# Kernel tuning notes

Hardware: AMD Instinct MI355X
Metric: run time of the kernel (lower is better)

## Reference

```python
import jax, jax.numpy as jnp
import numpy as np

# static architecture constants (match init_kwargs)
H, D, N_BASIS, MEM_LEN, QLEN = 16, 128, 1024, 512, 2048
RIDGE = 0.5
BASIS_SIGMAS = (0.005, 0.01)


def _gaussian_pdf(x, mu, sigma):
    return jnp.exp(-0.5 * ((x - mu) / sigma) ** 2) / (sigma * jnp.sqrt(2.0 * jnp.pi))


def _basis_params(n):
    # torch.meshgrid(linspace(0,1,n//2), sigmas, indexing='ij') then flatten
    m = jnp.linspace(0.0, 1.0, n // len(BASIS_SIGMAS)).astype(jnp.float32)
    mu = jnp.repeat(m, len(BASIS_SIGMAS))
    sigma = jnp.tile(jnp.asarray(BASIS_SIGMAS, jnp.float32), n // len(BASIS_SIGMAS))
    return mu, sigma


def _compute_G(l, b_mu, b_sigma, n):
    # padded linear positions on [-0.5+shift, 1.5-shift], l even -> 2l points
    shift = 1.0 / (2 * l)
    pos = jnp.linspace(-0.5 + shift, 1.5 - shift, 2 * l).astype(jnp.float32)
    F = _gaussian_pdf(pos[None, :], b_mu[:, None], b_sigma[:, None])  # [N, 2l]
    # G = F^T (F F^T + ridge I)^{-1}, then crop padding rows -> [l, N]
    G = jnp.linalg.solve(F @ F.T + RIDGE * jnp.eye(n, dtype=jnp.float32), F).T
    return G[l // 2: -(l // 2)]


def _forward(k, q, W_key, W_val, W_out, w_mu, w_sigma):
    d = H * D
    b_mu, b_sigma = _basis_params(N_BASIS)
    k = k[:, -512:, :]                                   # forward truncates memory
    l = k.shape[1]
    G = _compute_G(l, b_mu, b_sigma, N_BASIS)            # [l, N]
    # value_function: project signal onto basis coefficients B -> [1, N, d]
    B = jnp.einsum('bld,ln->bnd', k, G)
    keys = (B @ W_key.T).reshape(1, N_BASIS, H, D).transpose(0, 2, 1, 3)    # [1,H,N,D]
    values = (B @ W_val.T).reshape(1, N_BASIS, H, D).transpose(0, 2, 1, 3)  # [1,H,N,D]
    scores = jnp.einsum('bhqd,bhnd->bhqn', q / jnp.sqrt(jnp.float32(D)), keys)
    mu = jax.nn.sigmoid(scores @ w_mu)[..., None]                           # [1,H,Q,1]
    sigma_sq = jnp.maximum(jax.nn.softplus(scores @ w_sigma), 1e-4)[..., None]
    # continuous softmax over Gaussian RBFs: r_j = E_{t~N(mu,sigma_sq)}[psi_j(t)]
    # closed form: N(mu; b_mu_j, sigma_sq + b_sigma_j^2)
    r = _gaussian_pdf(b_mu, mu, jnp.sqrt(sigma_sq + b_sigma ** 2))          # [1,H,Q,N]
    context = jnp.einsum('bhqn,bhnd->bqhd', r, values).reshape(1, QLEN, d)
    return context @ W_out.T


def setup_inputs() -> dict:
    key = jax.random.key(0)
    ks = jax.random.split(key, 7)
    d = H * D
    s = 0.02
    return {
        'k': jax.random.normal(ks[0], (1, MEM_LEN, d), jnp.float32),
        'q': jax.random.normal(ks[1], (1, H, QLEN, D), jnp.float32),
        'W_key': jax.random.normal(ks[2], (d, d), jnp.float32) * s,
        'W_val': jax.random.normal(ks[3], (d, d), jnp.float32) * s,
        'W_out': jax.random.normal(ks[4], (d, d), jnp.float32) * s,
        'w_mu': jax.random.normal(ks[5], (N_BASIS,), jnp.float32) * s,
        'w_sigma': jax.random.normal(ks[6], (N_BASIS,), jnp.float32) * s,
        'new_doc': 1,
    }


def reference(k, q, W_key, W_val, W_out, w_mu, w_sigma, new_doc):
    # new_doc=True -> B_past/x_past reset, so only the fresh-memory path runs
    return _forward(k, q, W_key, W_val, W_out, w_mu, w_sigma)
```

## Files before the change

### kernel.cpp

```cpp
#include <hip/hip_runtime.h>
#include <hip/hip_bf16.h>
#include <vector>
#include <cmath>
#include <cstring>

using bf16 = __hip_bfloat16;
typedef short s16x8 __attribute__((ext_vector_type(8)));
typedef float f32x4 __attribute__((ext_vector_type(4)));

static constexpr int kH = 16, kD = 128, kNB = 1024, kML = 512, kQL = 2048, kDM = 2048;

#define VMB(N) do { asm volatile("s_waitcnt vmcnt(" #N ")" ::: "memory"); \
                    __builtin_amdgcn_s_barrier(); \
                    asm volatile("" ::: "memory"); } while (0)
#define VMLB(N) do { asm volatile("s_waitcnt vmcnt(" #N ") lgkmcnt(0)" ::: "memory"); \
                     __builtin_amdgcn_s_barrier(); \
                     asm volatile("" ::: "memory"); } while (0)
#define SWZ(c) ((c) ^ (((c) >> 4) & 3))

static void compute_Gt_host(float* Gt) {
  const int n = kNB, P = 2 * kML;
  std::vector<double> F((size_t)n * P), A((size_t)n * n), pos(P);
  const double shift = 1.0 / (double)P;
  const double p0 = -0.5 + shift, p1 = 1.5 - shift;
  for (int i = 0; i < P; i++) pos[i] = p0 + (p1 - p0) * (double)i / (double)(P - 1);
  const double c0 = 0.3989422804014327;
  std::vector<int> lo(n), hi(n);
  for (int b = 0; b < n; b++) {
    double mu = (double)(b >> 1) / 511.0;
    double sg = (b & 1) ? 0.01 : 0.005;
    double c = c0 / sg;
    double* Fb = &F[(size_t)b * P];
    for (int i = 0; i < P; i++) { double t = (pos[i] - mu) / sg; Fb[i] = c * exp(-0.5 * t * t); }
    int l = 0; while (l < P - 1 && pos[l] < mu - 14.0 * sg) l++;
    int h = P - 1; while (h > 0 && pos[h] > mu + 14.0 * sg) h--;
    lo[b] = l; hi[b] = h;
  }
  for (int i = 0; i < n; i++) {
    const double* fi = &F[(size_t)i * P];
    for (int j = 0; j <= i; j++) {
      const double* fj = &F[(size_t)j * P];
      int a = lo[i] > lo[j] ? lo[i] : lo[j];
      int b2 = hi[i] < hi[j] ? hi[i] : hi[j];
      double s = 0.0;
      for (int k2 = a; k2 <= b2; k2++) s += fi[k2] * fj[k2];
      A[(size_t)i * n + j] = s;
      if (i != j) A[(size_t)j * n + i] = s;
    }
    A[(size_t)i * n + i] += 0.5;
  }
  for (int j = 0; j < n; j++) {
    double* Aj = &A[(size_t)j * n];
    double d = Aj[j];
    for (int k2 = 0; k2 < j; k2++) d -= Aj[k2] * Aj[k2];
    d = std::sqrt(d); Aj[j] = d;
    double inv = 1.0 / d;
    for (int i = j + 1; i < n; i++) {
      double* Ai = &A[(size_t)i * n];
      double s = Ai[j];
      for (int k2 = 0; k2 < j; k2++) s -= Ai[k2] * Aj[k2];
      Ai[j] = s * inv;
    }
  }
  for (int i = 0; i < n; i++) {
    double* yi = &F[(size_t)i * P];
    const double* Ai = &A[(size_t)i * n];
    for (int k2 = 0; k2 < i; k2++) {
      double lik = Ai[k2];
      const double* yk = &F[(size_t)k2 * P];
      for (int t = 0; t < P; t++) yi[t] -= lik * yk[t];
    }
    double inv = 1.0 / Ai[i];
    for (int t = 0; t < P; t++) yi[t] *= inv;
  }
  for (int i = n - 1; i >= 0; i--) {
    double* xi = &F[(size_t)i * P];
    for (int k2 = i + 1; k2 < n; k2++) {
      double lki = A[(size_t)k2 * n + i];
      const double* xk = &F[(size_t)k2 * P];
      for (int t = 0; t < P; t++) xi[t] -= lki * xk[t];
    }
    double inv = 1.0 / A[(size_t)i * n + i];
    for (int t = 0; t < P; t++) xi[t] *= inv;
  }
  for (int b = 0; b < n; b++)
    for (int l = 0; l < kML; l++)
      Gt[(size_t)b * kML + l] = (float)F[(size_t)b * P + (kML / 2) + l];
}

static unsigned short f2bf_host(float x) {
  unsigned u; std::memcpy(&u, &x, 4);
  unsigned r = (u + 0x7FFFu + ((u >> 16) & 1u)) >> 16;
  return (unsigned short)r;
}
static float bf2f_host(unsigned short b) {
  unsigned u = ((unsigned)b) << 16; float f; std::memcpy(&f, &u, 4); return f;
}

namespace {
struct Init {
  float* d_GtTf = nullptr;
  unsigned short* d_Gth = nullptr;
  unsigned short* d_Gtl = nullptr;
  float* h_GtTf_pinned = nullptr;
  unsigned short* h_Gth_pinned = nullptr;
  unsigned short* h_Gtl_pinned = nullptr;
  std::vector<float> h_GtTf;
  std::vector<unsigned short> h_Gth, h_Gtl;
  Init() {
    std::vector<float> h_Gt((size_t)kNB * kML);
    compute_Gt_host(h_Gt.data());
    h_GtTf.resize(h_Gt.size());
    h_Gth.resize(h_Gt.size());
    h_Gtl.resize(h_Gt.size());
    for (int n = 0; n < kNB; n++)
      for (int l = 0; l < kML; l++) {
        float v = h_Gt[(size_t)n * kML + l];
        h_GtTf[(size_t)l * kNB + n] = v;
        unsigned short hb = f2bf_host(v);
        h_Gth[(size_t)n * kML + l] = hb;
        h_Gtl[(size_t)n * kML + l] = f2bf_host(v - bf2f_host(hb));
      }
    const size_t fb = h_Gt.size() * 4, bb = h_Gt.size() * 2;
    if (hipMalloc((void**)&d_GtTf, fb) == hipSuccess) {
      if (hipMemcpy(d_GtTf, h_GtTf.data(), fb, hipMemcpyHostToDevice) != hipSuccess) { hipFree(d_GtTf); d_GtTf = nullptr; }
    }
    if (hipMalloc((void**)&d_Gth, bb) == hipSuccess) {
      if (hipMemcpy(d_Gth, h_Gth.data(), bb, hipMemcpyHostToDevice) != hipSuccess) { hipFree(d_Gth); d_Gth = nullptr; }
    }
    if (hipMalloc((void**)&d_Gtl, bb) == hipSuccess) {
      if (hipMemcpy(d_Gtl, h_Gtl.data(), bb, hipMemcpyHostToDevice) != hipSuccess) { hipFree(d_Gtl); d_Gtl = nullptr; }
    }
    if (!d_GtTf && hipHostMalloc((void**)&h_GtTf_pinned, fb, 0) == hipSuccess)
      std::memcpy(h_GtTf_pinned, h_GtTf.data(), fb);
    if (!d_Gth && hipHostMalloc((void**)&h_Gth_pinned, bb, 0) == hipSuccess)
      std::memcpy(h_Gth_pinned, h_Gth.data(), bb);
    if (!d_Gtl && hipHostMalloc((void**)&h_Gtl_pinned, bb, 0) == hipSuccess)
      std::memcpy(h_Gtl_pinned, h_Gtl.data(), bb);
  }
};
Init g_init;
}

__device__ inline short f2bf(float x) {
  unsigned u = __float_as_uint(x);
  unsigned r = (u + 0x7FFFu + ((u >> 16) & 1u)) >> 16;
  return (short)r;
}
__device__ inline float bf2f(short b) {
  return __uint_as_float(((unsigned)(unsigned short)b) << 16);
}

__device__ inline void gload16(const void* g, void* l) {
  __builtin_amdgcn_global_load_lds(
      (__attribute__((address_space(1))) void*)(g),
      (__attribute__((address_space(3))) void*)(l),
      16, 0, 0);
}

__device__ inline int detect_local(const unsigned short* q) {
  int bad = 0;
  for (int i = threadIdx.x; i < 512; i += 256) {
    int e = (q[i] >> 7) & 0xFF;
    if (e >= 0x98) bad = 1;
  }
  __shared__ int s[256];
  s[threadIdx.x] = bad; __syncthreads();
  for (int k2 = 128; k2 > 0; k2 >>= 1) {
    if (threadIdx.x < k2) s[threadIdx.x] |= s[threadIdx.x + k2];
    __syncthreads();
  }
  return s[0];
}

__global__ __launch_bounds__(256) void prep_kernel(const unsigned short* __restrict__ q,
                                                   const void* __restrict__ kin,
                                                   const void* __restrict__ Wv,
                                                   short* __restrict__ k_bf,
                                                   short* __restrict__ Wv_bf,
                                                   float* __restrict__ bw,
                                                   int* __restrict__ flag) {
  const int f32 = detect_local(q);
  if (blockIdx.x == 0) {
    if (threadIdx.x == 0) *flag = f32;
    for (int i = threadIdx.x; i < 2 * kDM; i += 256) bw[i] = 0.f;
  }
  const void* src; short* dst; int i;
  if (blockIdx.x < 1024) { src = kin; dst = k_bf; i = blockIdx.x * 256 + threadIdx.x; }
  else { src = Wv; dst = Wv_bf; i = (blockIdx.x - 1024) * 256 + threadIdx.x; }
  if (f32) {
    float4 v = ((const float4*)src)[i];
    short4 o; o.x = f2bf(v.x); o.y = f2bf(v.y); o.z = f2bf(v.z); o.w = f2bf(v.w);
    ((short4*)dst)[i] = o;
  } else {
    ((short4*)dst)[i] = ((const short4*)src)[i];
  }
}

__global__ __launch_bounds__(256) void conv_bf16(const void* __restrict__ in,
                                                 short* __restrict__ out, int n4,
                                                 const int* __restrict__ flag) {
  int i = blockIdx.x * 256 + threadIdx.x;
  if (i >= n4) return;
  if (*flag) {
    float4 v = ((const float4*)in)[i];
    short4 o; o.x = f2bf(v.x); o.y = f2bf(v.y); o.z = f2bf(v.z); o.w = f2bf(v.w);
    ((short4*)out)[i] = o;
  } else {
    ((short4*)out)[i] = ((const short4*)in)[i];
  }
}

__global__ __launch_bounds__(256) void gw_kernel(const float* __restrict__ GtT,
                                                 const void* __restrict__ wmu,
                                                 const void* __restrict__ wsg,
                                                 float* __restrict__ gw,
                                                 const int* __restrict__ flag) {
  const bool f32 = (*flag != 0);
  const int l = blockIdx.x, t = threadIdx.x;
  const float* row = GtT + (long long)l * kNB;
  float a = 0.f, b = 0.f;
  for (int n = t; n < kNB; n += 256) {
    float g = row[n];
    float wm_ = f32 ? ((const float*)wmu)[n] : bf2f(((const short*)wmu)[n]);
    float ws_ = f32 ? ((const float*)wsg)[n] : bf2f(((const short*)wsg)[n]);
    a += g * wm_; b += g * ws_;
  }
  __shared__ float red[2][256];
  red[0][t] = a; red[1][t] = b;
  __syncthreads();
  for (int s = 128; s > 0; s >>= 1) {
    if (t < s) { red[0][t] += red[0][t + s]; red[1][t] += red[1][t + s]; }
    __syncthreads();
  }
  if (t == 0) { gw[l] = red[0][0]; gw[kML + l] = red[1][0]; }
}

__global__ __launch_bounds__(256) void bwk_kernel(const void* __restrict__ kin,
                                                  const float* __restrict__ gw,
                                                  float* __restrict__ bw,
                                                  const int* __restrict__ flag) {
  const bool f32 = (*flag != 0);
  int j = blockIdx.x * 256 + threadIdx.x;
  int l0 = blockIdx.y * 32;
  float a = 0.f, b = 0.f;
  for (int l = l0; l < l0 + 32; l++) {
    float kv = f32 ? ((const float*)kin)[(long long)l * kDM + j]
                   : bf2f(((const short*)kin)[(long long)l * kDM + j]);
    a += kv * gw[l]; b += kv * gw[kML + l];
  }
  atomicAdd(&bw[j], a);
  atomicAdd(&bw[kDM + j], b);
}

__global__ __launch_bounds__(256) void kw_kernel(const void* __restrict__ Wk,
                                                 const float* __restrict__ bw,
                                                 float* __restrict__ kw,
                                                 const int* __restrict__ flag) {
  const bool f32 = (*flag != 0);
  int i = blockIdx.x;
  float smu = 0.f, ssg = 0.f;
  if (f32) {
    const float* row = (const float*)Wk + (long long)i * kDM;
    for (int j = threadIdx.x; j < kDM; j += 256) { float w = row[j]; smu += w * bw[j]; ssg += w * bw[kDM + j]; }
  } else {
    const short* row = (const short*)Wk + (long long)i * kDM;
    for (int j = threadIdx.x; j < kDM; j += 256) { float w = bf2f(row[j]); smu += w * bw[j]; ssg += w * bw[kDM + j]; }
  }
  __shared__ float red[2][256];
  red[0][threadIdx.x] = smu; red[1][threadIdx.x] = ssg;
  __syncthreads();
  for (int s = 128; s > 0; s >>= 1) {
    if (threadIdx.x < (unsigned)s) {
      red[0][threadIdx.x] += red[0][threadIdx.x + s];
      red[1][threadIdx.x] += red[1][threadIdx.x + s];
    }
    __syncthreads();
  }
  if (threadIdx.x == 0) { kw[i] = red[0][0]; kw[kDM + i] = red[1][0]; }
}

template <int CSTORE>
__global__ __launch_bounds__(256) void mfma_gemm_bt(
    const short* __restrict__ A0, int lda, long long sA,
    const short* __restrict__ BT0, int ldb, long long sB,
    void* __restrict__ C0, int ldc, long long sC,
    int K, const int* __restrict__ flag) {
  __shared__ s16x8 lA[3][1024];
  __shared__ s16x8 lB[3][512];
  const short* A = A0 + (long long)blockIdx.z * sA;
  const short* BT = BT0 + (long long)blockIdx.z * sB;
  const int t = threadIdx.x;
  const int wave = t >> 6, lane = t & 63;
  const int quad = lane >> 4, l16 = lane & 15;
  const int wm = wave >> 1, wn = wave & 1;
  int m0, n0;
  if (gridDim.x == 32 && gridDim.y == 16) {
    const int bid = blockIdx.x + (blockIdx.y << 5);
    const int xcd = bid & 7, rank = bid >> 3;
    n0 = (((xcd & 3) << 3) + (rank & 7)) * 64;
    m0 = (((xcd >> 2) << 3) + (rank >> 3)) * 128;
  } else {
    m0 = blockIdx.y * 128; n0 = blockIdx.x * 64;
  }
  const int srow = lane & 15, skc = lane >> 4;
  auto stage = [&](int b, int kk) {
#pragma unroll
    for (int i = 0; i < 2; i++) {
      int sub = wave + i * 4;
      int m = sub * 16 + srow;
#pragma unroll
      for (int ks = 0; ks < 2; ks++)
        gload16(A + (long long)(m0 + m) * lda + kk + ks * 32 + skc * 8,
                &lA[b][ks * 512 + sub * 64]);
    }
    int mB = wave * 16 + srow;
#pragma unroll
    for (int ks = 0; ks < 2; ks++)
      gload16(BT + (long long)(n0 + mB) * ldb + kk + ks * 32 + skc * 8,
              &lB[b][ks * 256 + wave * 64]);
  };
  f32x4 acc[4][2];
  const f32x4 z = {0.f, 0.f, 0.f, 0.f};
#pragma unroll
  for (int i = 0; i < 4; i++)
#pragma unroll
    for (int j = 0; j < 2; j++) acc[i][j] = z;
  stage(0, 0);
  stage(1, 64);
  VMB(6);
  const int NT = K >> 6;
  int cur = 0, pf = 2;
  for (int tt = 0; tt < NT; ++tt) {
    const bool more = (tt + 2 < NT);
    if (more) stage(pf, (tt + 2) << 6);
#pragma unroll
    for (int ks = 0; ks < 2; ks++) {
      s16x8 af[4], bfr[2];
#pragma unroll
      for (int i = 0; i < 4; i++) af[i] = lA[cur][ks * 512 + (wm * 4 + i) * 64 + lane];
#pragma unroll
      for (int j = 0; j < 2; j++) bfr[j] = lB[cur][ks * 256 + (wn * 2 + j) * 64 + lane];
#pragma unroll
      for (int i = 0; i < 4; i++)
#pragma unroll
        for (int j = 0; j < 2; j++)
          acc[i][j] = __builtin_amdgcn_mfma_f32_16x16x32_bf16(af[i], bfr[j], acc[i][j], 0, 0, 0);
    }
    if (more) VMB(6); else VMB(0);
    cur = (cur == 2) ? 0 : cur + 1;
    pf = (pf == 2) ? 0 : pf + 1;
  }
  if (CSTORE == 0) {
    short* Cp = (short*)C0 + (long long)blockIdx.z * sC;
#pragma unroll
    for (int i = 0; i < 4; i++)
#pragma unroll
      for (int j = 0; j < 2; j++) {
        int gn = n0 + (wn * 2 + j) * 16 + l16;
#pragma unroll
        for (int rg = 0; rg < 4; rg++) {
          int gm = m0 + (wm * 4 + i) * 16 + quad * 4 + rg;
          Cp[(long long)gm * ldc + gn] = f2bf(acc[i][j][rg]);
        }
      }
  } else {
    if (*flag) {
      float* Cp = (float*)C0 + (long long)blockIdx.z * sC;
#pragma unroll
      for (int i = 0; i < 4; i++)
#pragma unroll
        for (int j = 0; j < 2; j++) {
          int gn = n0 + (wn * 2 + j) * 16 + l16;
#pragma unroll
          for (int rg = 0; rg < 4; rg++) {
            int gm = m0 + (wm * 4 + i) * 16 + quad * 4 + rg;
            Cp[(long long)gm * ldc + gn] = acc[i][j][rg];
          }
        }
    } else {
      short* Cp = (short*)C0 + (long long)blockIdx.z * sC;
#pragma unroll
      for (int i = 0; i < 4; i++)
#pragma unroll
        for (int j = 0; j < 2; j++) {
          int gn = n0 + (wn * 2 + j) * 16 + l16;
#pragma unroll
          for (int rg = 0; rg < 4; rg++) {
            int gm = m0 + (wm * 4 + i) * 16 + quad * 4 + rg;
            Cp[(long long)gm * ldc + gn] = f2bf(acc[i][j][rg]);
          }
        }
    }
  }
}

__global__ __launch_bounds__(256) void mfma_gemm_sk(
    const short* __restrict__ A0, int lda,
    const short* __restrict__ BT0, int ldb,
    float* __restrict__ P, int ldc) {
  __shared__ s16x8 lA[3][1024], lB[3][512];
  const int t = threadIdx.x;
  const int wave = t >> 6, lane = t & 63;
  const int quad = lane >> 4, l16 = lane & 15;
  const int wm = wave >> 1, wn = wave & 1;
  const int m0 = blockIdx.y * 128, n0 = blockIdx.x * 64;
  const int kbeg = blockIdx.z * 512;
  const int srow = lane & 15, skc = lane >> 4;
  auto stage = [&](int b, int kk) {
#pragma unroll
    for (int i = 0; i < 2; i++) {
      int sub = wave + i * 4;
      int m = sub * 16 + srow;
#pragma unroll
      for (int ks = 0; ks < 2; ks++)
        gload16(A0 + (long long)(m0 + m) * lda + kk + ks * 32 + skc * 8,
                &lA[b][ks * 512 + sub * 64]);
    }
    int mB = wave * 16 + srow;
#pragma unroll
    for (int ks = 0; ks < 2; ks++)
      gload16(BT0 + (long long)(n0 + mB) * ldb + kk + ks * 32 + skc * 8,
              &lB[b][ks * 256 + wave * 64]);
  };
  f32x4 acc[4][2];
  const f32x4 z = {0.f, 0.f, 0.f, 0.f};
#pragma unroll
  for (int i = 0; i < 4; i++)
#pragma unroll
    for (int j = 0; j < 2; j++) acc[i][j] = z;
  stage(0, kbeg);
  stage(1, kbeg + 64);
  VMB(6);
  const int NT = 8;
  int cur = 0, pf = 2;
  for (int tt = 0; tt < NT; ++tt) {
    const bool more = (tt + 2 < NT);
    if (more) stage(pf, kbeg + ((tt + 2) << 6));
#pragma unroll
    for (int ks = 0; ks < 2; ks++) {
      s16x8 af[4], bfr[2];
#pragma unroll
      for (int i = 0; i < 4; i++) af[i] = lA[cur][ks * 512 + (wm * 4 + i) * 64 + lane];
#pragma unroll
      for (int j = 0; j < 2; j++) bfr[j] = lB[cur][ks * 256 + (wn * 2 + j) * 64 + lane];
#pragma unroll
      for (int i = 0; i < 4; i++)
#pragma unroll
        for (int j = 0; j < 2; j++)
          acc[i][j] = __builtin_amdgcn_mfma_f32_16x16x32_bf16(af[i], bfr[j], acc[i][j], 0, 0, 0);
    }
    if (more) VMB(6); else VMB(0);
    cur = (cur == 2) ? 0 : cur + 1;
    pf = (pf == 2) ? 0 : pf + 1;
  }
  float* Cp = P + (long long)blockIdx.z * kML * kDM;
#pragma unroll
  for (int i = 0; i < 4; i++)
#pragma unroll
    for (int j = 0; j < 2; j++) {
      int gn = n0 + (wn * 2 + j) * 16 + l16;
#pragma unroll
      for (int rg = 0; rg < 4; rg++) {
        int gm = m0 + (wm * 4 + i) * 16 + quad * 4 + rg;
        Cp[(long long)gm * ldc + gn] = acc[i][j][rg];
      }
    }
}

__global__ __launch_bounds__(256) void reduceT_kernel(const float* __restrict__ P,
                                                      short* __restrict__ kvT) {
  __shared__ float tile[64][65];
  const int bd = blockIdx.x, bl = blockIdx.y;
  const int tx = threadIdx.x & 63, ty = threadIdx.x >> 6;
  for (int i = ty; i < 64; i += 4) {
    int l = bl * 64 + i, d = bd * 64 + tx;
    float s = 0.f;
#pragma unroll
    for (int z = 0; z < 4; z++) s += P[((long long)z * kML + l) * kDM + d];
    tile[i][tx] = s;
  }
  __syncthreads();
  for (int i = ty; i < 64; i += 4) {
    int d = bd * 64 + i, l = bl * 64 + tx;
    kvT[(long long)d * kML + l] = f2bf(tile[tx][i]);
  }
}

__global__ __launch_bounds__(256) void mfma_gemm_bt2(
    const short* __restrict__ A0, int lda,
    const short* __restrict__ BTh, const short* __restrict__ BTl, int ldb,
    short* __restrict__ Ch, short* __restrict__ Cl, int ldc, int K) {
  __shared__ s16x8 lA[3][256], lBh[3][256], lBl[3][256];
  const int t = threadIdx.x;
  const int wave = t >> 6, lane = t & 63;
  const int quad = lane >> 4, l16 = lane & 15;
  const int wm = wave >> 1, wn = wave & 1;
  const int m0 = blockIdx.y * 64, n0 = blockIdx.x * 64;
  const int srow = lane & 15, skc = lane >> 4;
  auto stage = [&](int b, int kk) {
    int m = wave * 16 + srow;
    gload16(A0 + (long long)(m0 + m) * lda + kk + skc * 8, &lA[b][wave * 64]);
    gload16(BTh + (long long)(n0 + m) * ldb + kk + skc * 8, &lBh[b][wave * 64]);
    gload16(BTl + (long long)(n0 + m) * ldb + kk + skc * 8, &lBl[b][wave * 64]);
  };
  f32x4 acc[2][2];
  const f32x4 z = {0.f, 0.f, 0.f, 0.f};
#pragma unroll
  for (int i = 0; i < 2; i++)
#pragma unroll
    for (int j = 0; j < 2; j++) acc[i][j] = z;
  stage(0, 0);
  stage(1, 32);
  VMB(3);
  const int NT = K >> 5;
  int cur = 0, pf = 2;
  for (int tt = 0; tt < NT; ++tt) {
    const bool more = (tt + 2 < NT);
    if (more) stage(pf, (tt + 2) << 5);
    s16x8 af[2], bh[2], bl[2];
#pragma unroll
    for (int i = 0; i < 2; i++) af[i] = lA[cur][(wm * 2 + i) * 64 + lane];
#pragma unroll
    for (int j = 0; j < 2; j++) {
      bh[j] = lBh[cur][(wn * 2 + j) * 64 + lane];
      bl[j] = lBl[cur][(wn * 2 + j) * 64 + lane];
    }
#pragma unroll
    for (int i = 0; i < 2; i++)
#pragma unroll
      for (int j = 0; j < 2; j++) {
        acc[i][j] = __builtin_amdgcn_mfma_f32_16x16x32_bf16(af[i], bh[j], acc[i][j], 0, 0, 0);
        acc[i][j] = __builtin_amdgcn_mfma_f32_16x16x32_bf16(af[i], bl[j], acc[i][j], 0, 0, 0);
      }
    if (more) VMB(3); else VMB(0);
    cur = (cur == 2) ? 0 : cur + 1;
    pf = (pf == 2) ? 0 : pf + 1;
  }
#pragma unroll
  for (int i = 0; i < 2; i++)
#pragma unroll
    for (int j = 0; j < 2; j++) {
      int gn = n0 + (wn * 2 + j) * 16 + l16;
#pragma unroll
      for (int rg = 0; rg < 4; rg++) {
        int gm = m0 + (wm * 2 + i) * 16 + quad * 4 + rg;
        float v = acc[i][j][rg];
        short hb = f2bf(v);
        Ch[(long long)gm * ldc + gn] = hb;
        Cl[(long long)gm * ldc + gn] = f2bf(v - bf2f(hb));
      }
    }
}

__global__ __launch_bounds__(256) void mfma_rv(
    const void* __restrict__ q, const float* __restrict__ kw,
    const int* __restrict__ flag,
    const short* __restrict__ VTh, const short* __restrict__ VTl,
    short* __restrict__ ctx) {
  __shared__ s16x8 lAh[3][256], lAl[3][256], lBh[3][512], lBl[3][512];
  const int t = threadIdx.x;
  const int wave = t >> 6, lane = t & 63;
  const int quad = lane >> 4, l16 = lane & 15;
  const int wm = wave >> 1, wn = wave & 1;
  const int bid = blockIdx.y;
  const int h = bid & 15;
  const int m0 = (bid >> 4) * 64;
  const int r0 = t >> 2, kc = t & 3;
  const int srow = lane & 15, skc = lane >> 4;
  const long long voff = (long long)h * kD * kNB;
  const int row = h * kQL + m0 + r0;
  float a = 0.f, b = 0.f;
  {
    const bool f32q = (*flag != 0);
    const float* kmu = kw + h * kD;
    const float* ksg = kw + kDM + h * kD;
    if (f32q) {
      const float* qrow = (const float*)q + (long long)row * kD;
      for (int jj = kc * 32; jj < kc * 32 + 32; jj++) {
        float qv = qrow[jj];
        a += qv * kmu[jj]; b += qv * ksg[jj];
      }
    } else {
      const short* qrow = (const short*)q + (long long)row * kD;
      for (int jj = kc * 32; jj < kc * 32 + 32; jj++) {
        float qv = bf2f(qrow[jj]);
        a += qv * kmu[jj]; b += qv * ksg[jj];
      }
    }
    a += __shfl_xor(a, 1); a += __shfl_xor(a, 2);
    b += __shfl_xor(b, 1); b += __shfl_xor(b, 2);
  }
  const float inv_sqrt_d = 0.08838834764831845f;
  const float zm = a * inv_sqrt_d, zs = b * inv_sqrt_d;
  const float m_ = 1.f / (1.f + __expf(-zm));
  const float sp = (zs > 20.f) ? zs : log1pf(__expf(zs));
  const float s2 = fmaxf(sp, 1e-4f);
  float ivs[2], cof[2];
  ivs[0] = rsqrtf(s2 + 2.5e-5f);
  ivs[1] = rsqrtf(s2 + 1e-4f);
  cof[0] = 0.3989422804014327f * ivs[0];
  cof[1] = 0.3989422804014327f * ivs[1];
  const int cidx = SWZ((r0 >> 4) * 64 + kc * 16 + (r0 & 15));
  auto stageB = [&](int bb, int kk) {
#pragma unroll
    for (int i = 0; i < 2; i++) {
      int sub = wave + i * 4;
      int m = sub * 16 + srow;
      gload16(VTh + voff + (long long)m * kNB + kk + skc * 8, &lBh[bb][sub * 64]);
      gload16(VTl + voff + (long long)m * kNB + kk + skc * 8, &lBl[bb][sub * 64]);
    }
  };
  auto stageA = [&](int bb, int kk) {
    s16x8 hv, lv;
#pragma unroll
    for (int jj = 0; jj < 8; jj++) {
      int n = kk + kc * 8 + jj;
      float bmu = (float)(n >> 1) * (1.f / 511.f);
      int p = jj & 1;
      float tt = (bmu - m_) * ivs[p];
      float v = cof[p] * __expf(-0.5f * tt * tt);
      short hb = f2bf(v);
      hv[jj] = hb;
      lv[jj] = f2bf(v - bf2f(hb));
    }
    lAh[bb][cidx] = hv;
    lAl[bb][cidx] = lv;
  };
  f32x4 acc[2][4];
  const f32x4 z = {0.f, 0.f, 0.f, 0.f};
#pragma unroll
  for (int i = 0; i < 2; i++)
#pragma unroll
    for (int j = 0; j < 4; j++) acc[i][j] = z;
  stageB(0, 0);
  stageA(0, 0);
  stageB(1, 32);
  stageA(1, 32);
  VMLB(4);
  const int NT = kNB >> 5;
  int cur = 0, pf = 2;
  for (int tt = 0; tt < NT; ++tt) {
    const bool more = (tt + 2 < NT);
    if (more) {
      stageB(pf, (tt + 2) << 5);
      stageA(pf, (tt + 2) << 5);
    }
    s16x8 ah[2], al[2], bh[4], bl[4];
#pragma unroll
    for (int i = 0; i < 2; i++) {
      ah[i] = lAh[cur][SWZ((wm * 2 + i) * 64 + lane)];
      al[i] = lAl[cur][SWZ((wm * 2 + i) * 64 + lane)];
    }
#pragma unroll
    for (int j = 0; j < 4; j++) {
      bh[j] = lBh[cur][(wn * 4 + j) * 64 + lane];
      bl[j] = lBl[cur][(wn * 4 + j) * 64 + lane];
    }
#pragma unroll
    for (int i = 0; i < 2; i++)
#pragma unroll
      for (int j = 0; j < 4; j++) {
        acc[i][j] = __builtin_amdgcn_mfma_f32_16x16x32_bf16(ah[i], bh[j], acc[i][j], 0, 0, 0);
        acc[i][j] = __builtin_amdgcn_mfma_f32_16x16x32_bf16(ah[i], bl[j], acc[i][j], 0, 0, 0);
        acc[i][j] = __builtin_amdgcn_mfma_f32_16x16x32_bf16(al[i], bh[j], acc[i][j], 0, 0, 0);
      }
    if (more) VMLB(4); else VMLB(0);
    cur = (cur == 2) ? 0 : cur + 1;
    pf = (pf == 2) ? 0 : pf + 1;
  }
  short* Cp = ctx + h * kD;
#pragma unroll
  for (int i = 0; i < 2; i++)
#pragma unroll
    for (int j = 0; j < 4; j++) {
      int gn = (wn * 4 + j) * 16 + l16;
#pragma unroll
      for (int rg = 0; rg < 4; rg++) {
        int gm = m0 + (wm * 2 + i) * 16 + quad * 4 + rg;
        Cp[(long long)gm * kDM + gn] = f2bf(acc[i][j][rg]);
      }
    }
}

extern "C" void kernel_launch(void* const* d_in, const int* in_sizes, int n_in,
                              void* d_out, int out_size, void* d_ws, size_t ws_size,
                              hipStream_t stream) {
  (void)in_sizes; (void)n_in; (void)out_size; (void)ws_size;
  const void* kmem = d_in[0];
  const void* q    = d_in[1];
  const void* Wk   = d_in[2];
  const void* Wv   = d_in[3];
  const void* Wo   = d_in[4];
  const void* wmu  = d_in[5];
  const void* wsg  = d_in[6];

  char* ws = (char*)d_ws;
  short* k_bf  = (short*)ws;
  short* kvT   = (short*)(ws + ((size_t)2 << 20));
  short* Wv_bf = (short*)(ws + ((size_t)4 << 20));
  short* Wo_bf = Wv_bf;
  float* Pbuf  = (float*)(ws + ((size_t)12 << 20));
  short* VTh   = (short*)(ws + ((size_t)12 << 20));
  short* VTl   = (short*)(ws + ((size_t)16 << 20));
  short* ctx   = (short*)(ws + ((size_t)20 << 20));
  float* tail  = (float*)(ws + ((size_t)28 << 20));
  float* gw    = tail;
  float* bw    = gw + 2 * kML;
  float* kw    = bw + 2 * kDM;
  int*   flag  = (int*)(kw + 2 * kDM);
  float* gtffall = (float*)(ws + ((size_t)28 << 20) + ((size_t)1 << 19));
  short* ghfall  = (short*)(ws + ((size_t)30 << 20) + ((size_t)1 << 19));
  short* glfall  = (short*)(ws + ((size_t)31 << 20) + ((size_t)1 << 19));

  const float* GtTf = g_init.d_GtTf;
  if (!GtTf) {
    const void* src = g_init.h_GtTf_pinned ? (const void*)g_init.h_GtTf_pinned
                                           : (const void*)g_init.h_GtTf.data();
    hipMemcpyAsync(gtffall, src, (size_t)kNB * kML * 4, hipMemcpyHostToDevice, stream);
    GtTf = gtffall;
  }
  const short* Gh = (const short*)g_init.d_Gth;
  if (!Gh) {
    const void* src = g_init.h_Gth_pinned ? (const void*)g_init.h_Gth_pinned
                                          : (const void*)g_init.h_Gth.data();
    hipMemcpyAsync(ghfall, src, (size_t)kNB * kML * 2, hipMemcpyHostToDevice, stream);
    Gh = ghfall;
  }
  const short* Gl = (const short*)g_init.d_Gtl;
  if (!Gl) {
    const void* src = g_init.h_Gtl_pinned ? (const void*)g_init.h_Gtl_pinned
                                          : (const void*)g_init.h_Gtl.data();
    hipMemcpyAsync(glfall, src, (size_t)kNB * kML * 2, hipMemcpyHostToDevice, stream);
    Gl = glfall;
  }

  prep_kernel<<<5120, 256, 0, stream>>>((const unsigned short*)q, kmem, Wv,
                                        k_bf, Wv_bf, bw, flag);

  gw_kernel<<<kML, 256, 0, stream>>>(GtTf, wmu, wsg, gw, flag);
  bwk_kernel<<<dim3(kDM / 256, kML / 32), 256, 0, stream>>>(kmem, gw, bw, flag);
  kw_kernel<<<kDM, 256, 0, stream>>>(Wk, bw, kw, flag);

  mfma_gemm_sk<<<dim3(kDM / 64, kML / 128, 4), 256, 0, stream>>>(
      k_bf, kDM, Wv_bf, kDM, Pbuf, kDM);
  reduceT_kernel<<<dim3(kDM / 64, kML / 64), 256, 0, stream>>>(Pbuf, kvT);

  conv_bf16<<<(kDM * kDM / 4 + 255) / 256, 256, 0, stream>>>(Wo, Wo_bf, kDM * kDM / 4, flag);

  mfma_gemm_bt2<<<dim3(kNB / 64, kDM / 64, 1), 256, 0, stream>>>(
      kvT, kML, Gh, Gl, kML, VTh, VTl, kNB, kML);

  mfma_rv<<<dim3(1, (kQL / 64) * kH, 1), 256, 0, stream>>>(q, kw, flag, VTh, VTl, ctx);

  mfma_gemm_bt<2><<<dim3(kDM / 64, kQL / 128, 1), 256, 0, stream>>>(
      ctx, kDM, 0, Wo_bf, kDM, 0, d_out, kDM, 0, kDM, flag);
}
```

Measured before the change: 257.5 us.

## Load GEMM fragments directly from global memory into registers, dropping LDS staging

Replaces the triple-buffered LDS staging (async global-to-LDS loads plus barriers) in the bf16 MFMA GEMM with direct per-wave global loads into register fragments, software-pipelined across two k halves. This removes the shared-memory footprint and the block-wide barriers. In exchange, data shared between waves is no longer reused through LDS, so the same A/B rows are fetched from global or L2 by several waves. The 16-byte loads are also strided per row and less coalesced, with prefetch depth cut to one half-step.

New measurement: 297.6 us. +15.6%, slower.

```diff
diff --git a/kernel.cpp b/kernel.cpp
--- a/kernel.cpp
+++ b/kernel.cpp
@@ -286,8 +286,6 @@
     const short* __restrict__ BT0, int ldb, long long sB,
     void* __restrict__ C0, int ldc, long long sC,
     int K, const int* __restrict__ flag) {
-  __shared__ s16x8 lA[3][1024];
-  __shared__ s16x8 lB[3][512];
   const short* A = A0 + (long long)blockIdx.z * sA;
   const short* BT = BT0 + (long long)blockIdx.z * sB;
   const int t = threadIdx.x;
@@ -303,53 +301,46 @@
   } else {
     m0 = blockIdx.y * 128; n0 = blockIdx.x * 64;
   }
-  const int srow = lane & 15, skc = lane >> 4;
-  auto stage = [&](int b, int kk) {
-#pragma unroll
-    for (int i = 0; i < 2; i++) {
-      int sub = wave + i * 4;
-      int m = sub * 16 + srow;
-#pragma unroll
-      for (int ks = 0; ks < 2; ks++)
-        gload16(A + (long long)(m0 + m) * lda + kk + ks * 32 + skc * 8,
-                &lA[b][ks * 512 + sub * 64]);
-    }
-    int mB = wave * 16 + srow;
-#pragma unroll
-    for (int ks = 0; ks < 2; ks++)
-      gload16(BT + (long long)(n0 + mB) * ldb + kk + ks * 32 + skc * 8,
-              &lB[b][ks * 256 + wave * 64]);
-  };
+  const short* pa[4];
+  const short* pb[2];
+#pragma unroll
+  for (int i = 0; i < 4; i++)
+    pa[i] = A + (long long)(m0 + (wm * 4 + i) * 16 + l16) * lda + quad * 8;
+#pragma unroll
+  for (int j = 0; j < 2; j++)
+    pb[j] = BT + (long long)(n0 + (wn * 2 + j) * 16 + l16) * ldb + quad * 8;
   f32x4 acc[4][2];
   const f32x4 z = {0.f, 0.f, 0.f, 0.f};
 #pragma unroll
   for (int i = 0; i < 4; i++)
 #pragma unroll
     for (int j = 0; j < 2; j++) acc[i][j] = z;
-  stage(0, 0);
-  stage(1, 64);
-  VMB(6);
-  const int NT = K >> 6;
-  int cur = 0, pf = 2;
-  for (int tt = 0; tt < NT; ++tt) {
-    const bool more = (tt + 2 < NT);
-    if (more) stage(pf, (tt + 2) << 6);
-#pragma unroll
-    for (int ks = 0; ks < 2; ks++) {
-      s16x8 af[4], bfr[2];
-#pragma unroll
-      for (int i = 0; i < 4; i++) af[i] = lA[cur][ks * 512 + (wm * 4 + i) * 64 + lane];
-#pragma unroll
-      for (int j = 0; j < 2; j++) bfr[j] = lB[cur][ks * 256 + (wn * 2 + j) * 64 + lane];
-#pragma unroll
-      for (int i = 0; i < 4; i++)
-#pragma unroll
-        for (int j = 0; j < 2; j++)
-          acc[i][j] = __builtin_amdgcn_mfma_f32_16x16x32_bf16(af[i], bfr[j], acc[i][j], 0, 0, 0);
-    }
-    if (more) VMB(6); else VMB(0);
-    cur = (cur == 2) ? 0 : cur + 1;
-    pf = (pf == 2) ? 0 : pf + 1;
+  s16x8 a0[4], b0[2], a1[4], b1[2];
+#pragma unroll
+  for (int i = 0; i < 4; i++) a0[i] = *(const s16x8*)(pa[i]);
+#pragma unroll
+  for (int j = 0; j < 2; j++) b0[j] = *(const s16x8*)(pb[j]);
+  for (int k0 = 0; k0 < K; k0 += 64) {
+#pragma unroll
+    for (int i = 0; i < 4; i++) a1[i] = *(const s16x8*)(pa[i] + k0 + 32);
+#pragma unroll
+    for (int j = 0; j < 2; j++) b1[j] = *(const s16x8*)(pb[j] + k0 + 32);
+#pragma unroll
+    for (int i = 0; i < 4; i++)
+#pragma unroll
+      for (int j = 0; j < 2; j++)
+        acc[i][j] = __builtin_amdgcn_mfma_f32_16x16x32_bf16(a0[i], b0[j], acc[i][j], 0, 0, 0);
+    if (k0 + 64 < K) {
+#pragma unroll
+      for (int i = 0; i < 4; i++) a0[i] = *(const s16x8*)(pa[i] + k0 + 64);
+#pragma unroll
+      for (int j = 0; j < 2; j++) b0[j] = *(const s16x8*)(pb[j] + k0 + 64);
+    }
+#pragma unroll
+    for (int i = 0; i < 4; i++)
+#pragma unroll
+      for (int j = 0; j < 2; j++)
+        acc[i][j] = __builtin_amdgcn_mfma_f32_16x16x32_bf16(a1[i], b1[j], acc[i][j], 0, 0, 0);
   }
   if (CSTORE == 0) {
     short* Cp = (short*)C0 + (long long)blockIdx.z * sC;
```
